# Kernel tuning notes

Hardware: AMD Instinct MI355X
Metric: run time of the kernel (lower is better)

## Reference

```python
import jax, jax.numpy as jnp
import numpy as np

B, T, V, C, H, W = 8, 20, 6, 512, 7, 7
NC = 8  # num_classes
F_LOCAL = C * H * W        # 25088
F_GLOBAL = 2 * C * H * W   # 50176


def setup_inputs() -> dict:
    key = jax.random.key(0)
    ks = jax.random.split(key, 8)
    feats = jax.random.uniform(ks[0], (B, T, V, C, H, W), dtype=jnp.float32)
    W_local = jax.random.normal(ks[1], (V, F_LOCAL, C), dtype=jnp.float32) * 0.01
    b_local = jnp.zeros((V, C), dtype=jnp.float32)
    W_global = jax.random.normal(ks[2], (V, F_GLOBAL, C), dtype=jnp.float32) * 0.01
    b_global = jnp.zeros((V, C), dtype=jnp.float32)
    W_final = jax.random.normal(ks[3], (F_GLOBAL, NC), dtype=jnp.float32) * 0.01
    b_final = jnp.zeros((NC,), dtype=jnp.float32)
    W_time = jax.random.normal(ks[4], (T * NC, NC), dtype=jnp.float32) * 0.01
    b_time = jnp.zeros((NC,), dtype=jnp.float32)
    return {
        "feats": feats,
        "W_local": W_local, "b_local": b_local,
        "W_global": W_global, "b_global": b_global,
        "W_final": W_final, "b_final": b_final,
        "W_time": W_time, "b_time": b_time,
    }


def reference(feats, W_local, b_local, W_global, b_global,
              W_final, b_final, W_time, b_time):
    # feats: [B, T, V, C, H, W]
    Bn, Tn, Vn, Cn, Hn, Wn = feats.shape
    flat = feats.reshape(Bn, Tn, Vn, -1)                     # [B,T,V,C*H*W]
    # per-view local attention weights over channels
    w = jax.nn.sigmoid(jnp.einsum('btvf,vfc->btvc', flat, W_local) + b_local)
    w_norm = w / w.sum(axis=-1, keepdims=True)               # normalize over channels
    # channel-weighted multi-view aggregation (fused form of the double loop)
    agg = jnp.einsum('btvchw,btvc->btchw', feats, w_norm)    # [B,T,C,H,W]
    # global context: cat(local, aggregated) on channel dim, per view
    agg_b = jnp.broadcast_to(agg[:, :, None], feats.shape)   # [B,T,V,C,H,W]
    gflat = jnp.concatenate([feats, agg_b], axis=3).reshape(Bn, Tn, Vn, -1)
    r = jax.nn.sigmoid(jnp.einsum('btvf,vfc->btvc', gflat, W_global) + b_global)
    fw = w * r
    fw_norm = fw / fw.sum(axis=-1, keepdims=True)
    refined = jnp.einsum('btvchw,btvc->btchw', feats, fw_norm)  # [B,T,C,H,W]
    final_rep = jnp.concatenate([refined, agg], axis=2).reshape(Bn, Tn, -1)
    frame_out = final_rep @ W_final + b_final                # [B,T,NC]
    out = frame_out.reshape(Bn, -1) @ W_time + b_time        # [B,NC]
    return out
```

## Files before the change

kernel.cpp:

```cpp
#include <hip/hip_runtime.h>

#define F_LOC 25088
#define CDIM 512
#define VN 6
#define MN 160
#define HWN 49
#define NCLS 8
#define KSPLIT 16
#define KCHUNK 1568
#define NSTEP 49
#define ARS (VN * F_LOC)

typedef __attribute__((ext_vector_type(8))) short short8;
typedef __attribute__((ext_vector_type(4))) float f32x4;
typedef unsigned short u16;

__device__ __forceinline__ u16 f2bf(float f) {
  union { float f; unsigned u; } x; x.f = f;
  unsigned r = x.u + 0x7fffu + ((x.u >> 16) & 1u);
  return (u16)(r >> 16);
}
__device__ __forceinline__ float sigf(float x) { return 1.0f / (1.0f + __expf(-x)); }

__global__ void k_initframe(float* __restrict__ frame, const float* __restrict__ bf) {
  int i = blockIdx.x * blockDim.x + threadIdx.x;
  if (i < MN * NCLS) frame[i] = bf[i & 7];
}

__device__ __forceinline__ void gemm_core(
    const float* __restrict__ Ab, int a_rs,
    const float* __restrict__ Wp,
    float* __restrict__ op,
    u16* __restrict__ lds, int t) {
  const int lane = t & 63;
  const int l15 = lane & 15;
  const int kg = lane >> 4;

  f32x4 acc[10];
#pragma unroll
  for (int i = 0; i < 10; ++i) acc[i] = (f32x4)(0.0f);

  float4 areg[5];
  float bv[8], bvn[8];
#pragma unroll
  for (int p = 0; p < 5; ++p) {
    int i = t + p * 256, row = i >> 3, q = i & 7;
    areg[p] = *(const float4*)(Ab + (size_t)row * a_rs + q * 4);
  }
#pragma unroll
  for (int j = 0; j < 8; ++j) bv[j] = Wp[(size_t)(kg * 8 + j) * CDIM];

  for (int s = 0; s < NSTEP; ++s) {
    u16* buf = lds + (s & 1) * 6400;
#pragma unroll
    for (int p = 0; p < 5; ++p) {
      int i = t + p * 256, row = i >> 3, q = i & 7;
      ushort4 o;
      o.x = f2bf(areg[p].x); o.y = f2bf(areg[p].y);
      o.z = f2bf(areg[p].z); o.w = f2bf(areg[p].w);
      *(ushort4*)(buf + row * 40 + q * 4) = o;
    }
    __syncthreads();
    if (s < NSTEP - 1) {
#pragma unroll
      for (int p = 0; p < 5; ++p) {
        int i = t + p * 256, row = i >> 3, q = i & 7;
        areg[p] = *(const float4*)(Ab + (size_t)row * a_rs + (s + 1) * 32 + q * 4);
      }
#pragma unroll
      for (int j = 0; j < 8; ++j) bvn[j] = Wp[(size_t)((s + 1) * 32 + kg * 8 + j) * CDIM];
    }
    short8 bfrag;
#pragma unroll
    for (int j = 0; j < 8; ++j) bfrag[j] = (short)f2bf(bv[j]);
#pragma unroll
    for (int mt = 0; mt < 10; ++mt) {
      short8 af = *(const short8*)(buf + (l15 + 16 * mt) * 40 + kg * 8);
      acc[mt] = __builtin_amdgcn_mfma_f32_16x16x32_bf16(af, bfrag, acc[mt], 0, 0, 0);
    }
#pragma unroll
    for (int j = 0; j < 8; ++j) bv[j] = bvn[j];
  }
#pragma unroll
  for (int mt = 0; mt < 10; ++mt)
#pragma unroll
    for (int i = 0; i < 4; ++i) {
      int m = mt * 16 + kg * 4 + i;
      op[(size_t)m * (VN * CDIM)] = acc[mt][i];
    }
}

__global__ __launch_bounds__(256, 3) void k_gemm12(
    const float* __restrict__ feats, const float* __restrict__ Wl,
    const float* __restrict__ Wgl, float* __restrict__ wpart, float* __restrict__ rpart) {
  __shared__ u16 lds[2 * 6400];
  int bid = blockIdx.x;
  int sub = bid >= 768 ? 1 : 0;
  int b = bid - sub * 768;
  int g = b % 96, cb = b / 96;
  int v = g / KSPLIT, ks = g % KSPLIT;
  int t = threadIdx.x;
  int wv = t >> 6, l15 = t & 15;
  int c = cb * 64 + wv * 16 + l15;
  const float* Ab = feats + (size_t)v * F_LOC + (size_t)ks * KCHUNK;
  const float* W = sub ? Wgl : Wl;
  long long wvs = sub ? (long long)2 * F_LOC * CDIM : (long long)F_LOC * CDIM;
  const float* Wp = W + (size_t)v * wvs + (size_t)ks * KCHUNK * CDIM + c;
  float* op = (sub ? rpart : wpart) + (size_t)ks * MN * (VN * CDIM) + (size_t)v * CDIM + c;
  gemm_core(Ab, ARS, Wp, op, lds, t);
}

__global__ __launch_bounds__(256, 3) void k_gemm3(
    const float* __restrict__ agg, const float* __restrict__ Wgl, float* __restrict__ rpart) {
  __shared__ u16 lds[2 * 6400];
  int b = blockIdx.x;
  int g = b % 96, cb = b / 96;
  int v = g / KSPLIT, ks = g % KSPLIT;
  int t = threadIdx.x;
  int wv = t >> 6, l15 = t & 15;
  int c = cb * 64 + wv * 16 + l15;
  const float* Ab = agg + (size_t)ks * KCHUNK;
  const float* Wp = Wgl + (size_t)F_LOC * CDIM + (size_t)v * (2ll * F_LOC * CDIM) +
                    (size_t)ks * KCHUNK * CDIM + c;
  float* op = rpart + (size_t)(KSPLIT + ks) * MN * (VN * CDIM) + (size_t)v * CDIM + c;
  gemm_core(Ab, F_LOC, Wp, op, lds, t);
}

__global__ void k_wnorm(const float* __restrict__ part, const float* __restrict__ bias,
                        float* __restrict__ w, float* __restrict__ wn, int nslot) {
  int v = blockIdx.x, m = blockIdx.y, t = threadIdx.x;
  const size_t slot_stride = (size_t)MN * VN * CDIM;
  size_t base = (size_t)m * (VN * CDIM) + v * CDIM;
  float s0 = bias[v * CDIM + t], s1 = bias[v * CDIM + t + 256];
  for (int j = 0; j < nslot; ++j) {
    s0 += part[j * slot_stride + base + t];
    s1 += part[j * slot_stride + base + t + 256];
  }
  s0 = sigf(s0); s1 = sigf(s1);
  w[base + t] = s0; w[base + t + 256] = s1;
  __shared__ float red[256];
  red[t] = s0 + s1;
  __syncthreads();
  for (int o = 128; o > 0; o >>= 1) { if (t < o) red[t] += red[t + o]; __syncthreads(); }
  float inv = 1.0f / red[0];
  wn[base + t] = s0 * inv; wn[base + t + 256] = s1 * inv;
}

__global__ void k_fwnorm(const float* __restrict__ part, const float* __restrict__ bias,
                         const float* __restrict__ w, float* __restrict__ fwn, int nslot) {
  int v = blockIdx.x, m = blockIdx.y, t = threadIdx.x;
  const size_t slot_stride = (size_t)MN * VN * CDIM;
  size_t base = (size_t)m * (VN * CDIM) + v * CDIM;
  float s0 = bias[v * CDIM + t], s1 = bias[v * CDIM + t + 256];
  for (int j = 0; j < nslot; ++j) {
    s0 += part[j * slot_stride + base + t];
    s1 += part[j * slot_stride + base + t + 256];
  }
  float f0 = w[base + t] * sigf(s0);
  float f1 = w[base + t + 256] * sigf(s1);
  __shared__ float red[256];
  red[t] = f0 + f1;
  __syncthreads();
  for (int o = 128; o > 0; o >>= 1) { if (t < o) red[t] += red[t + o]; __syncthreads(); }
  float inv = 1.0f / red[0];
  fwn[base + t] = f0 * inv; fwn[base + t + 256] = f1 * inv;
}

__global__ void k_aggregate(const float* __restrict__ feats, const float* __restrict__ wn,
                            float* __restrict__ aggf, const float* __restrict__ Wf,
                            float* __restrict__ frame, int wf_off) {
  int m = blockIdx.y;
  int cbase = blockIdx.x * 64;
  int t = threadIdx.x;
  float p[8] = {0, 0, 0, 0, 0, 0, 0, 0};
  for (int idx = t; idx < 64 * HWN; idx += 256) {
    int cl = idx / HWN;
    int hw = idx - cl * HWN;
    int c = cbase + cl;
    float val = 0.0f;
#pragma unroll
    for (int v = 0; v < VN; ++v)
      val += feats[(((size_t)m * VN + v) * CDIM + c) * HWN + hw] * wn[((size_t)m * VN + v) * CDIM + c];
    if (aggf) aggf[(size_t)m * F_LOC + c * HWN + hw] = val;
    const float* wr = Wf + ((size_t)wf_off + c * HWN + hw) * NCLS;
#pragma unroll
    for (int n = 0; n < NCLS; ++n) p[n] += val * wr[n];
  }
  __shared__ float red[256];
  for (int n = 0; n < NCLS; ++n) {
    red[t] = p[n];
    __syncthreads();
    for (int o = 128; o > 0; o >>= 1) { if (t < o) red[t] += red[t + o]; __syncthreads(); }
    if (t == 0) atomicAdd(&frame[m * NCLS + n], red[0]);
    __syncthreads();
  }
}

__global__ void k_out(const float* __restrict__ frame, const float* __restrict__ Wt,
                      const float* __restrict__ bt, float* __restrict__ out) {
  int t = threadIdx.x;
  int b = t >> 3, n = t & 7;
  float acc = bt[n];
  for (int k = 0; k < MN; ++k) acc += frame[b * MN + k] * Wt[k * NCLS + n];
  out[t] = acc;
}

extern "C" void kernel_launch(void* const* d_in, const int* in_sizes, int n_in,
                              void* d_out, int out_size, void* d_ws, size_t ws_size,
                              hipStream_t stream) {
  const float* feats    = (const float*)d_in[0];
  const float* W_local  = (const float*)d_in[1];
  const float* b_local  = (const float*)d_in[2];
  const float* W_global = (const float*)d_in[3];
  const float* b_global = (const float*)d_in[4];
  const float* W_final  = (const float*)d_in[5];
  const float* b_final  = (const float*)d_in[6];
  const float* W_time   = (const float*)d_in[7];
  const float* b_time   = (const float*)d_in[8];
  float* out = (float*)d_out;

  char* ws = (char*)d_ws;
  size_t off = 0;
  float* aggf   = (float*)(ws + off); off += (size_t)MN * F_LOC * 4;
  float* wpart  = (float*)(ws + off); off += (size_t)KSPLIT * MN * VN * CDIM * 4;
  float* rpart  = (float*)(ws + off); off += (size_t)2 * KSPLIT * MN * VN * CDIM * 4;
  float* wbuf   = (float*)(ws + off); off += (size_t)MN * VN * CDIM * 4;
  float* wnorm  = (float*)(ws + off); off += (size_t)MN * VN * CDIM * 4;
  float* fwnorm = (float*)(ws + off); off += (size_t)MN * VN * CDIM * 4;
  float* frame  = (float*)(ws + off); off += 8192;

  k_initframe<<<(MN * NCLS + 255) / 256, 256, 0, stream>>>(frame, b_final);

  k_gemm12<<<1536, 256, 0, stream>>>(feats, W_local, W_global, wpart, rpart);
  k_wnorm<<<dim3(6, 160), 256, 0, stream>>>(wpart, b_local, wbuf, wnorm, KSPLIT);
  k_aggregate<<<dim3(8, 160), 256, 0, stream>>>(feats, wnorm, aggf, W_final, frame, F_LOC);
  k_gemm3<<<768, 256, 0, stream>>>(aggf, W_global, rpart);
  k_fwnorm<<<dim3(6, 160), 256, 0, stream>>>(rpart, b_global, wbuf, fwnorm, 2 * KSPLIT);
  k_aggregate<<<dim3(8, 160), 256, 0, stream>>>(feats, fwnorm, nullptr, W_final, frame, 0);
  k_out<<<1, 64, 0, stream>>>(frame, W_time, b_time, out);
}
```

Baseline: 406.2 us.

## Share feats A-tile across W_local and W_global GEMMs, split M, deepen B prefetch

k_gemm12 now gives each block one 80-row half of M and computes both the W_local and the first half of the W_global projections from a single staged A tile, so feats is converted and staged once for both weights instead of once per GEMM. The B operand is now prefetched two k-steps ahead through an unrolled even/odd register pair. The LDS row pitch shrinks from 40 to 36 elements. The shared core is templated over M tiles and the number of weight matrices, which adds accumulator registers (two sets of five) and may put pressure on occupancy under the 3-block launch bound.

```diff
diff --git a/kernel.cpp b/kernel.cpp
--- a/kernel.cpp
+++ b/kernel.cpp
@@ -27,92 +27,126 @@
   if (i < MN * NCLS) frame[i] = bf[i & 7];
 }
 
-__device__ __forceinline__ void gemm_core(
+#define GSTEP(S, BCUR, PH, DO_A, DO_B)                                                   \
+  {                                                                                      \
+    u16* buf = lds + (PH) * LDSB;                                                        \
+    _Pragma("unroll") for (int p = 0; p < NLD; ++p) {                                    \
+      int i = t + p * 256;                                                               \
+      if (NLD * 256 == NF4 || i < NF4) {                                                 \
+        int row = i >> 3, q = i & 7;                                                     \
+        ushort4 o;                                                                       \
+        o.x = f2bf(areg[p].x); o.y = f2bf(areg[p].y);                                    \
+        o.z = f2bf(areg[p].z); o.w = f2bf(areg[p].w);                                    \
+        *(ushort4*)(buf + row * 36 + q * 4) = o;                                         \
+      }                                                                                  \
+    }                                                                                    \
+    __syncthreads();                                                                     \
+    if (DO_A) {                                                                          \
+      _Pragma("unroll") for (int p = 0; p < NLD; ++p) {                                  \
+        int i = t + p * 256;                                                             \
+        if (NLD * 256 == NF4 || i < NF4) {                                               \
+          int row = i >> 3, q = i & 7;                                                   \
+          areg[p] = *(const float4*)(Ab + (size_t)row * a_rs + ((S) + 1) * 32 + q * 4);  \
+        }                                                                                \
+      }                                                                                  \
+    }                                                                                    \
+    short8 bfrag[NSUB];                                                                  \
+    _Pragma("unroll") for (int u = 0; u < NSUB; ++u)                                     \
+      _Pragma("unroll") for (int j = 0; j < 8; ++j)                                      \
+        bfrag[u][j] = (short)f2bf(BCUR[u][j]);                                           \
+    if (DO_B) {                                                                          \
+      _Pragma("unroll") for (int u = 0; u < NSUB; ++u)                                   \
+        _Pragma("unroll") for (int j = 0; j < 8; ++j)                                    \
+          BCUR[u][j] = Wp[u][(size_t)(((S) + 2) * 32 + kg * 8 + j) * CDIM];              \
+    }                                                                                    \
+    _Pragma("unroll") for (int mt = 0; mt < MT; ++mt) {                                  \
+      short8 af = *(const short8*)(buf + (l15 + 16 * mt) * 36 + kg * 8);                 \
+      _Pragma("unroll") for (int u = 0; u < NSUB; ++u)                                   \
+        acc[u][mt] = __builtin_amdgcn_mfma_f32_16x16x32_bf16(af, bfrag[u], acc[u][mt], 0, 0, 0); \
+    }                                                                                    \
+  }
+
+template <int MT, int NSUB>
+__device__ __forceinline__ void gemm_core2(
     const float* __restrict__ Ab, int a_rs,
-    const float* __restrict__ Wp,
-    float* __restrict__ op,
+    const float* __restrict__ W0, const float* __restrict__ W1,
+    float* __restrict__ op0, float* __restrict__ op1,
     u16* __restrict__ lds, int t) {
   const int lane = t & 63;
   const int l15 = lane & 15;
   const int kg = lane >> 4;
-
-  f32x4 acc[10];
-#pragma unroll
-  for (int i = 0; i < 10; ++i) acc[i] = (f32x4)(0.0f);
-
-  float4 areg[5];
-  float bv[8], bvn[8];
-#pragma unroll
-  for (int p = 0; p < 5; ++p) {
-    int i = t + p * 256, row = i >> 3, q = i & 7;
-    areg[p] = *(const float4*)(Ab + (size_t)row * a_rs + q * 4);
-  }
-#pragma unroll
-  for (int j = 0; j < 8; ++j) bv[j] = Wp[(size_t)(kg * 8 + j) * CDIM];
-
-  for (int s = 0; s < NSTEP; ++s) {
-    u16* buf = lds + (s & 1) * 6400;
-#pragma unroll
-    for (int p = 0; p < 5; ++p) {
-      int i = t + p * 256, row = i >> 3, q = i & 7;
-      ushort4 o;
-      o.x = f2bf(areg[p].x); o.y = f2bf(areg[p].y);
-      o.z = f2bf(areg[p].z); o.w = f2bf(areg[p].w);
-      *(ushort4*)(buf + row * 40 + q * 4) = o;
+  constexpr int NLD = (MT + 1) / 2;
+  constexpr int NF4 = MT * 128;
+  constexpr int LDSB = MT * 16 * 36;
+
+  f32x4 acc[NSUB][MT];
+#pragma unroll
+  for (int u = 0; u < NSUB; ++u)
+#pragma unroll
+    for (int i = 0; i < MT; ++i) acc[u][i] = (f32x4)(0.0f);
+
+  const float* Wp[2] = {W0, W1};
+  float4 areg[NLD];
+  float bE[NSUB][8], bO[NSUB][8];
+
+#pragma unroll
+  for (int p = 0; p < NLD; ++p) {
+    int i = t + p * 256;
+    if (NLD * 256 == NF4 || i < NF4) {
+      int row = i >> 3, q = i & 7;
+      areg[p] = *(const float4*)(Ab + (size_t)row * a_rs + q * 4);
     }
-    __syncthreads();
-    if (s < NSTEP - 1) {
-#pragma unroll
-      for (int p = 0; p < 5; ++p) {
-        int i = t + p * 256, row = i >> 3, q = i & 7;
-        areg[p] = *(const float4*)(Ab + (size_t)row * a_rs + (s + 1) * 32 + q * 4);
-      }
-#pragma unroll
-      for (int j = 0; j < 8; ++j) bvn[j] = Wp[(size_t)((s + 1) * 32 + kg * 8 + j) * CDIM];
-    }
-    short8 bfrag;
-#pragma unroll
-    for (int j = 0; j < 8; ++j) bfrag[j] = (short)f2bf(bv[j]);
-#pragma unroll
-    for (int mt = 0; mt < 10; ++mt) {
-      short8 af = *(const short8*)(buf + (l15 + 16 * mt) * 40 + kg * 8);
-      acc[mt] = __builtin_amdgcn_mfma_f32_16x16x32_bf16(af, bfrag, acc[mt], 0, 0, 0);
-    }
-#pragma unroll
-    for (int j = 0; j < 8; ++j) bv[j] = bvn[j];
-  }
-#pragma unroll
-  for (int mt = 0; mt < 10; ++mt)
-#pragma unroll
-    for (int i = 0; i < 4; ++i) {
-      int m = mt * 16 + kg * 4 + i;
-      op[(size_t)m * (VN * CDIM)] = acc[mt][i];
-    }
+  }
+#pragma unroll
+  for (int u = 0; u < NSUB; ++u)
+#pragma unroll
+    for (int j = 0; j < 8; ++j) bE[u][j] = Wp[u][(size_t)(kg * 8 + j) * CDIM];
+#pragma unroll
+  for (int u = 0; u < NSUB; ++u)
+#pragma unroll
+    for (int j = 0; j < 8; ++j) bO[u][j] = Wp[u][(size_t)(32 + kg * 8 + j) * CDIM];
+
+  for (int ss = 0; ss < 24; ++ss) {
+    int s = 2 * ss;
+    GSTEP(s, bE, 0, true, true);
+    GSTEP(s + 1, bO, 1, true, ss < 23);
+  }
+  GSTEP(48, bE, 0, false, false);
+
+#pragma unroll
+  for (int u = 0; u < NSUB; ++u) {
+    float* op = u ? op1 : op0;
+#pragma unroll
+    for (int mt = 0; mt < MT; ++mt)
+#pragma unroll
+      for (int i = 0; i < 4; ++i)
+        op[(size_t)(mt * 16 + kg * 4 + i) * (VN * CDIM)] = acc[u][mt][i];
+  }
 }
 
 __global__ __launch_bounds__(256, 3) void k_gemm12(
     const float* __restrict__ feats, const float* __restrict__ Wl,
     const float* __restrict__ Wgl, float* __restrict__ wpart, float* __restrict__ rpart) {
-  __shared__ u16 lds[2 * 6400];
+  __shared__ u16 lds[2 * 5 * 16 * 36];
   int bid = blockIdx.x;
-  int sub = bid >= 768 ? 1 : 0;
-  int b = bid - sub * 768;
-  int g = b % 96, cb = b / 96;
+  int cb = bid / 192;
+  int r = bid - cb * 192;
+  int ms = r / 96;
+  int g = r - ms * 96;
   int v = g / KSPLIT, ks = g % KSPLIT;
   int t = threadIdx.x;
   int wv = t >> 6, l15 = t & 15;
   int c = cb * 64 + wv * 16 + l15;
-  const float* Ab = feats + (size_t)v * F_LOC + (size_t)ks * KCHUNK;
-  const float* W = sub ? Wgl : Wl;
-  long long wvs = sub ? (long long)2 * F_LOC * CDIM : (long long)F_LOC * CDIM;
-  const float* Wp = W + (size_t)v * wvs + (size_t)ks * KCHUNK * CDIM + c;
-  float* op = (sub ? rpart : wpart) + (size_t)ks * MN * (VN * CDIM) + (size_t)v * CDIM + c;
-  gemm_core(Ab, ARS, Wp, op, lds, t);
+  const float* Ab = feats + (size_t)ms * 80 * ARS + (size_t)v * F_LOC + (size_t)ks * KCHUNK;
+  const float* W0 = Wl + (size_t)v * ((long long)F_LOC * CDIM) + (size_t)ks * KCHUNK * CDIM + c;
+  const float* W1 = Wgl + (size_t)v * (2ll * F_LOC * CDIM) + (size_t)ks * KCHUNK * CDIM + c;
+  size_t ob = ((size_t)ks * MN + (size_t)ms * 80) * (VN * CDIM) + (size_t)v * CDIM + c;
+  gemm_core2<5, 2>(Ab, ARS, W0, W1, wpart + ob, rpart + ob, lds, t);
 }
 
 __global__ __launch_bounds__(256, 3) void k_gemm3(
     const float* __restrict__ agg, const float* __restrict__ Wgl, float* __restrict__ rpart) {
-  __shared__ u16 lds[2 * 6400];
+  __shared__ u16 lds[2 * 10 * 16 * 36];
   int b = blockIdx.x;
   int g = b % 96, cb = b / 96;
   int v = g / KSPLIT, ks = g % KSPLIT;
@@ -122,8 +156,8 @@
   const float* Ab = agg + (size_t)ks * KCHUNK;
   const float* Wp = Wgl + (size_t)F_LOC * CDIM + (size_t)v * (2ll * F_LOC * CDIM) +
                     (size_t)ks * KCHUNK * CDIM + c;
-  float* op = rpart + (size_t)(KSPLIT + ks) * MN * (VN * CDIM) + (size_t)v * CDIM + c;
-  gemm_core(Ab, F_LOC, Wp, op, lds, t);
+  float* op = rpart + ((size_t)(KSPLIT + ks) * MN) * (VN * CDIM) + (size_t)v * CDIM + c;
+  gemm_core2<10, 1>(Ab, F_LOC, Wp, nullptr, op, nullptr, lds, t);
 }
 
 __global__ void k_wnorm(const float* __restrict__ part, const float* __restrict__ bias,
```

After: 501.2 us. 1.23x slower.
